# Kernel optimization log

Hardware: AMD Instinct MI355X
Metric: run time of the kernel (lower is better)

The kernel has to match this reference:

```python
import jax, jax.numpy as jnp
import numpy as np
from jax import lax

NUM_CHANNELS = 64
DILATION_DEPTH = 9
NUM_REPEAT = 2
KERNEL_SIZE = 3
DILATIONS = [2 ** d for d in range(DILATION_DEPTH)] * NUM_REPEAT  # 18 layers
B, T = 4, 32768


def causal_conv1d(x, w, b, dilation):
    # x: [B, Cin, T], w: [Cout, Cin, K], b: [Cout]
    # left-pad by (K-1)*dilation -> causal, output length T
    pad = (w.shape[-1] - 1) * dilation
    out = lax.conv_general_dilated(
        x, w, window_strides=(1,), padding=[(pad, 0)],
        rhs_dilation=(dilation,), dimension_numbers=("NCH", "OIH", "NCH"))
    return out + b[None, :, None]


def setup_inputs() -> dict:
    key = jax.random.key(0)
    ks = jax.random.split(key, 9)
    L, C = len(DILATIONS), NUM_CHANNELS
    s = 0.05
    return {
        "x": jax.random.normal(ks[0], (B, 1, T), dtype=jnp.float32),
        "in_w": jax.random.normal(ks[1], (C, 1, 1), dtype=jnp.float32) * s,
        "in_b": jax.random.normal(ks[2], (C,), dtype=jnp.float32) * s,
        "hid_w": jax.random.normal(ks[3], (L, 2 * C, C, KERNEL_SIZE), dtype=jnp.float32) * s,
        "hid_b": jax.random.normal(ks[4], (L, 2 * C), dtype=jnp.float32) * s,
        "res_w": jax.random.normal(ks[5], (L, C, C, 1), dtype=jnp.float32) * s,
        "res_b": jax.random.normal(ks[6], (L, C), dtype=jnp.float32) * s,
        "mix_w": jax.random.normal(ks[7], (1, L * C, 1), dtype=jnp.float32) * s,
        "mix_b": jax.random.normal(ks[8], (1,), dtype=jnp.float32) * s,
    }


def reference(x, in_w, in_b, hid_w, hid_b, res_w, res_b, mix_w, mix_b):
    C = NUM_CHANNELS
    out = causal_conv1d(x, in_w, in_b, 1)  # [B, C, T]
    skips = []
    for i, d in enumerate(DILATIONS):
        inp = out
        h = causal_conv1d(inp, hid_w[i], hid_b[i], d)  # [B, 2C, T]
        gated = jnp.tanh(h[:, :C]) * jax.nn.sigmoid(h[:, C:])  # [B, C, T]
        skips.append(gated)
        out = causal_conv1d(gated, res_w[i], res_b[i], 1) + inp
    skip_cat = jnp.concatenate(skips, axis=1)  # [B, L*C, T]
    return causal_conv1d(skip_cat, mix_w, mix_b, 1)  # [B, 1, T]
```

## Files before the change

kernel.cpp:

```cpp
#include <hip/hip_runtime.h>
#include <math.h>

#define T_LEN 32768
#define NB 4
#define NC 64
#define NL 18

typedef __attribute__((ext_vector_type(8))) short s16x8;
typedef __attribute__((ext_vector_type(4))) float f32x4;
#define MFMA_F16 __builtin_amdgcn_mfma_f32_16x16x32_f16

#define BAR_LGKM()                                                   \
    do {                                                             \
        asm volatile("s_waitcnt lgkmcnt(0)" ::: "memory");           \
        __builtin_amdgcn_s_barrier();                                \
        __builtin_amdgcn_sched_barrier(0);                           \
    } while (0)
#define BAR_VM(N)                                                    \
    do {                                                             \
        asm volatile("s_waitcnt vmcnt(%0) lgkmcnt(0)" ::             \
                         "i"(N) : "memory");                         \
        __builtin_amdgcn_s_barrier();                                \
        __builtin_amdgcn_sched_barrier(0);                           \
    } while (0)

__device__ inline unsigned short f2h(float f) {
    _Float16 h = (_Float16)f;
    return __builtin_bit_cast(unsigned short, h);
}
__device__ inline unsigned pack_h2(float a, float b) {
    return (unsigned)f2h(a) | ((unsigned)f2h(b) << 16);
}
__device__ inline float h2f(unsigned short u) {
    return (float)__builtin_bit_cast(_Float16, u);
}
__device__ inline float fast_sigmoid(float x) {
    return __builtin_amdgcn_rcpf(1.f + __expf(-x));
}
__device__ inline float fast_tanh(float x) {
    return 1.f - 2.f * __builtin_amdgcn_rcpf(1.f + __expf(2.f * x));
}

__global__ void prep_kernel(const float* __restrict__ hid_w,
                            const float* __restrict__ res_w,
                            const float* __restrict__ mix_b,
                            unsigned short* __restrict__ Wh,
                            unsigned short* __restrict__ Wr,
                            float* __restrict__ out,
                            float* __restrict__ zerobuf) {
    const int nW1 = NL * 128 * 192;
    const int nW2 = NL * 64 * 64;
    const int nOut = NB * T_LEN;
    const int total = nW1 + nW2 + nOut + 32;
    for (int gid = blockIdx.x * blockDim.x + threadIdx.x; gid < total;
         gid += gridDim.x * blockDim.x) {
        if (gid < nW1) {
            int K = gid % 192;
            int co = (gid / 192) & 127;
            int i = gid / (192 * 128);
            int kt = K >> 6, ci = K & 63;
            Wh[gid] = f2h(hid_w[((i * 128 + co) * 64 + ci) * 3 + kt]);
        } else if (gid < nW1 + nW2) {
            int q = gid - nW1;
            int c = q & 63, co = (q >> 6) & 63, i = q >> 12;
            Wr[q] = f2h(res_w[(i * 64 + co) * 64 + c]);
        } else if (gid < nW1 + nW2 + nOut) {
            out[gid - (nW1 + nW2)] = mix_b[0];
        } else {
            zerobuf[gid - (nW1 + nW2 + nOut)] = 0.f;
        }
    }
}

template <int DIL, bool FIRST, bool LAST>
__launch_bounds__(256, 4)
__global__ void layer_kernel(const unsigned short* __restrict__ actH,
                             unsigned short* __restrict__ outH,
                             const unsigned short* __restrict__ Wh,
                             const float* __restrict__ hb,
                             const unsigned short* __restrict__ Wr,
                             const float* __restrict__ rb,
                             const float* __restrict__ mw,
                             float* __restrict__ skip,
                             const float* __restrict__ zerobuf,
                             const float* __restrict__ x,
                             const float* __restrict__ in_w,
                             const float* __restrict__ in_b) {
    constexpr bool UNI = (DIL < 64);
    constexpr int R = UNI ? (64 + 2 * DIL) : 192;
    constexpr int SLOTS = R * 8;
    constexpr int JMAX = (SLOTS + 255) / 256;
    constexpr int GS_BASE = (UNI ? 128 : 0) * 128;
    constexpr int OUT_BASE = (UNI ? 0 : 64) * 128;
    constexpr int REG = 24576;

    __shared__ uint4 Xs[2 * 1536];
    __shared__ float Sk[256];
    char* lds = (char*)Xs;

    const int tid = threadIdx.x;
    const int w = tid >> 6;
    const int l = tid & 63;
    const int lo = l & 15;
    const int hi = l >> 4;
    const int b = blockIdx.y;
    const int tile = (blockIdx.x & 7) * 32 + (blockIdx.x >> 3);
    const int t0 = tile * 128;
    const int m0 = 16 * w;
    const int c0 = m0 + 4 * hi;

    const unsigned short* actB = actH + (size_t)b * T_LEN * NC;
    const float* xB = x + (size_t)b * T_LEN;

    s16x8 AH[2][6];
    s16x8 AR[2];
#pragma unroll
    for (int mt = 0; mt < 2; mt++) {
        const unsigned short* wp = Wh + (size_t)(m0 + 64 * mt + lo) * 192;
#pragma unroll
        for (int s = 0; s < 6; s++)
            AH[mt][s] = *(const s16x8*)(wp + 32 * s + 8 * hi);
    }
    if (!LAST) {
#pragma unroll
        for (int s = 0; s < 2; s++)
            AR[s] = *(const s16x8*)(Wr + (size_t)(m0 + lo) * 64 + 32 * s + 8 * hi);
    }
    float bA[4], bB[4], rbv[4];
#pragma unroll
    for (int r = 0; r < 4; r++) {
        bA[r] = hb[c0 + r];
        bB[r] = hb[64 + c0 + r];
        rbv[r] = LAST ? 0.f : rb[c0 + r];
    }
    const float4 mw4 = *(const float4*)(mw + c0);

    if (FIRST) {
#pragma unroll
        for (int sub = 0; sub < 2; sub++) {
            char* X = lds + sub * REG;
            const int tb = t0 + sub * 64;
#pragma unroll
            for (int j = 0; j < JMAX; j++) {
                int p = j * 256 + tid;
                if (p < SLOTS) {
                    int row = p >> 3, ch = p & 7;
                    int tg = tb + row - 2 * DIL;
                    unsigned uu[4] = {0u, 0u, 0u, 0u};
                    if (tg >= 0) {
                        float a = xB[tg];
#pragma unroll
                        for (int e = 0; e < 4; e++) {
                            float v0 = a * in_w[ch * 8 + 2 * e] + in_b[ch * 8 + 2 * e];
                            float v1 = a * in_w[ch * 8 + 2 * e + 1] + in_b[ch * 8 + 2 * e + 1];
                            uu[e] = pack_h2(v0, v1);
                        }
                    }
                    int byte = (row * 128 + ch * 16) ^ ((row & 7) << 4);
                    *(uint4*)(X + byte) = make_uint4(uu[0], uu[1], uu[2], uu[3]);
                }
            }
        }
    } else {
#pragma unroll
        for (int sub = 0; sub < 2; sub++) {
            char* X = lds + sub * REG;
            const int tb = t0 + sub * 64;
#pragma unroll
            for (int j = 0; j < JMAX; j++) {
                int s = (w * JMAX + j) * 64 + l;
                const void* src;
                if (s >= SLOTS) {
                    src = (const void*)(zerobuf + (s & 7) * 4);
                } else {
                    int row = s >> 3, ch = s & 7;
                    int chunk = ch ^ (row & 7);
                    int tg = tb + (UNI ? (row - 2 * DIL)
                                       : (((row >> 6) - 2) * DIL + (row & 63)));
                    src = (tg >= 0)
                              ? (const void*)(actB + (size_t)tg * 64 + chunk * 8)
                              : (const void*)(zerobuf + chunk * 4);
                }
                __builtin_amdgcn_global_load_lds(
                    (const __attribute__((address_space(1))) unsigned int*)src,
                    (__attribute__((address_space(3))) unsigned int*)(X +
                                                        (w * JMAX + j) * 1024),
                    16, 0, 0);
            }
        }
    }

#pragma unroll
    for (int sub = 0; sub < 2; sub++) {
        char* X = lds + sub * REG;
        const int tt0 = t0 + sub * 64;

        if (FIRST) {
            BAR_LGKM();
        } else if (sub == 0) {
            BAR_VM(JMAX);
        } else {
            BAR_VM(0);
        }

        f32x4 acc[2][4];
#pragma unroll
        for (int mt = 0; mt < 2; mt++)
#pragma unroll
            for (int nt = 0; nt < 4; nt++)
                acc[mt][nt] = (f32x4){0.f, 0.f, 0.f, 0.f};
#pragma unroll
        for (int s = 0; s < 6; s++) {
            const int tap = s >> 1, half = s & 1;
#pragma unroll
            for (int nt = 0; nt < 4; nt++) {
                int t = 16 * nt + lo;
                int row = UNI ? (t + tap * DIL) : (tap * 64 + t);
                int byte = (row * 128 + half * 64 + hi * 16) ^ ((row & 7) << 4);
                s16x8 bx = __builtin_bit_cast(s16x8, *(const uint4*)(X + byte));
                acc[0][nt] = MFMA_F16(AH[0][s], bx, acc[0][nt], 0, 0, 0);
                acc[1][nt] = MFMA_F16(AH[1][s], bx, acc[1][nt], 0, 0, 0);
            }
        }

        float4 inp[4];
        if (!LAST) {
#pragma unroll
            for (int nt = 0; nt < 4; nt++) {
                int t = 16 * nt + lo;
                int rowI = UNI ? (t + 2 * DIL) : (128 + t);
                int byteI = (rowI * 128 + c0 * 2) ^ ((rowI & 7) << 4);
                uint2 hv = *(const uint2*)(X + byteI);
                inp[nt] = make_float4(h2f((unsigned short)(hv.x & 0xffff)),
                                      h2f((unsigned short)(hv.x >> 16)),
                                      h2f((unsigned short)(hv.y & 0xffff)),
                                      h2f((unsigned short)(hv.y >> 16)));
            }
        }

        BAR_LGKM();

#pragma unroll
        for (int nt = 0; nt < 4; nt++) {
            float g[4];
#pragma unroll
            for (int r = 0; r < 4; r++) {
                float hA = acc[0][nt][r] + bA[r];
                float hB = acc[1][nt][r] + bB[r];
                g[r] = fast_tanh(hA) * fast_sigmoid(hB);
            }
            int t = 16 * nt + lo;
            if (!LAST) {
                int byte = (t * 128 + c0 * 2) ^ ((t & 7) << 4);
                *(uint2*)(X + GS_BASE + byte) =
                    make_uint2(pack_h2(g[0], g[1]), pack_h2(g[2], g[3]));
            }
            float sk = g[0] * mw4.x + g[1] * mw4.y + g[2] * mw4.z + g[3] * mw4.w;
            sk += __shfl_xor(sk, 16, 64);
            sk += __shfl_xor(sk, 32, 64);
            if (hi == 0) Sk[w * 64 + nt * 16 + lo] = sk;
        }
        BAR_LGKM();

        if (LAST) {
            if (tid < 64) {
                float s2 = Sk[tid] + Sk[64 + tid] + Sk[128 + tid] + Sk[192 + tid];
                skip[(size_t)b * T_LEN + tt0 + tid] += s2;
            }
            continue;
        }

        f32x4 acc2[4];
#pragma unroll
        for (int nt = 0; nt < 4; nt++) acc2[nt] = (f32x4){0.f, 0.f, 0.f, 0.f};
#pragma unroll
        for (int s = 0; s < 2; s++) {
#pragma unroll
            for (int nt = 0; nt < 4; nt++) {
                int t = 16 * nt + lo;
                int byte = (t * 128 + s * 64 + hi * 16) ^ ((t & 7) << 4);
                s16x8 bg = __builtin_bit_cast(
                    s16x8, *(const uint4*)(X + GS_BASE + byte));
                acc2[nt] = MFMA_F16(AR[s], bg, acc2[nt], 0, 0, 0);
            }
        }

        char* OutH = X + OUT_BASE;
#pragma unroll
        for (int nt = 0; nt < 4; nt++) {
            int t = 16 * nt + lo;
            float ox = acc2[nt][0] + rbv[0] + inp[nt].x;
            float oy = acc2[nt][1] + rbv[1] + inp[nt].y;
            float oz = acc2[nt][2] + rbv[2] + inp[nt].z;
            float ow = acc2[nt][3] + rbv[3] + inp[nt].w;
            int byteB = (t * 128 + c0 * 2) ^ ((t & 7) << 4);
            *(uint2*)(OutH + byteB) =
                make_uint2(pack_h2(ox, oy), pack_h2(oz, ow));
        }

        if (tid < 64) {
            float s2 = Sk[tid] + Sk[64 + tid] + Sk[128 + tid] + Sk[192 + tid];
            skip[(size_t)b * T_LEN + tt0 + tid] += s2;
        }
        BAR_LGKM();

        unsigned short* gH = outH + (size_t)b * T_LEN * NC + (size_t)tt0 * 64;
#pragma unroll
        for (int i = 0; i < 2; i++) {
            int u = i * 256 + tid;
            int t = u >> 3, ch = u & 7;
            uint4 v = *(const uint4*)(OutH + t * 128 + ((ch ^ (t & 7)) << 4));
            ((uint4*)gH)[u] = v;
        }
    }
}

extern "C" void kernel_launch(void* const* d_in, const int* in_sizes, int n_in,
                              void* d_out, int out_size, void* d_ws, size_t ws_size,
                              hipStream_t stream) {
    const float* x     = (const float*)d_in[0];
    const float* in_w  = (const float*)d_in[1];
    const float* in_b  = (const float*)d_in[2];
    const float* hid_w = (const float*)d_in[3];
    const float* hid_b = (const float*)d_in[4];
    const float* res_w = (const float*)d_in[5];
    const float* res_b = (const float*)d_in[6];
    const float* mix_w = (const float*)d_in[7];
    const float* mix_b = (const float*)d_in[8];
    float* out = (float*)d_out;

    const size_t actN = (size_t)NB * T_LEN * NC;
    unsigned short* H0 = (unsigned short*)d_ws;
    unsigned short* H1 = H0 + actN;
    unsigned short* Wh = H1 + actN;
    unsigned short* Wr = Wh + (size_t)NL * 128 * 192;
    float* zerobuf = (float*)(Wr + (size_t)NL * 64 * 64);

    prep_kernel<<<512, 256, 0, stream>>>(hid_w, res_w, mix_b, Wh, Wr, out,
                                         zerobuf);

    static const int dils[NL] = {1, 2, 4, 8, 16, 32, 64, 128, 256,
                                 1, 2, 4, 8, 16, 32, 64, 128, 256};
    const unsigned short* srcH = H0;
    unsigned short* dstH = H1;
    dim3 grid(T_LEN / 128, NB);

#define LL(D, F, L)                                                           \
    layer_kernel<D, F, L><<<grid, 256, 0, stream>>>(                          \
        srcH, dstH, Wh + (size_t)i * 128 * 192, hid_b + (size_t)i * 128,      \
        Wr + (size_t)i * 64 * 64, res_b + (size_t)i * 64,                     \
        mix_w + (size_t)i * 64, out, zerobuf, x, in_w, in_b)

    for (int i = 0; i < NL; i++) {
        if (i == 0) {
            LL(1, true, false);
        } else if (i == NL - 1) {
            LL(256, false, true);
        } else {
            switch (dils[i]) {
                case 1:   LL(1, false, false);   break;
                case 2:   LL(2, false, false);   break;
                case 4:   LL(4, false, false);   break;
                case 8:   LL(8, false, false);   break;
                case 16:  LL(16, false, false);  break;
                case 32:  LL(32, false, false);  break;
                case 64:  LL(64, false, false);  break;
                case 128: LL(128, false, false); break;
                case 256: LL(256, false, false); break;
            }
        }
        const unsigned short* tH = srcH; srcH = dstH; dstH = (unsigned short*)tH;
    }
#undef LL
}
```

Baseline: 373.9 us.

## Loop each block over the batch with double-buffered async staging

Each block now handles one 64-step time tile for all four batch elements instead of two time sub-tiles of one batch. While the current batch element is computed, the global-to-LDS load for the next one is issued into the other LDS buffer. Weight register loads are amortised over more work per block, and the grid shrinks from 1024 to 512 blocks. Extra barriers are added at the end of each iteration so the ping-pong buffer is safe to reuse, and the lower block count may reduce latency hiding.

```diff
diff --git a/kernel.cpp b/kernel.cpp
--- a/kernel.cpp
+++ b/kernel.cpp
@@ -103,14 +103,13 @@
     const int l = tid & 63;
     const int lo = l & 15;
     const int hi = l >> 4;
-    const int b = blockIdx.y;
-    const int tile = (blockIdx.x & 7) * 32 + (blockIdx.x >> 3);
-    const int t0 = tile * 128;
+    const int blk = blockIdx.x;
+    const int tile = (blk & 7) * 64 + (blk >> 3);
+    const int t0 = tile * 64;
     const int m0 = 16 * w;
     const int c0 = m0 + 4 * hi;
 
-    const unsigned short* actB = actH + (size_t)b * T_LEN * NC;
-    const float* xB = x + (size_t)b * T_LEN;
+    const float* xB0 = x;
 
     s16x8 AH[2][6];
     s16x8 AR[2];
@@ -135,73 +134,70 @@
     }
     const float4 mw4 = *(const float4*)(mw + c0);
 
-    if (FIRST) {
-#pragma unroll
-        for (int sub = 0; sub < 2; sub++) {
-            char* X = lds + sub * REG;
-            const int tb = t0 + sub * 64;
-#pragma unroll
-            for (int j = 0; j < JMAX; j++) {
-                int p = j * 256 + tid;
-                if (p < SLOTS) {
-                    int row = p >> 3, ch = p & 7;
-                    int tg = tb + row - 2 * DIL;
-                    unsigned uu[4] = {0u, 0u, 0u, 0u};
-                    if (tg >= 0) {
-                        float a = xB[tg];
-#pragma unroll
-                        for (int e = 0; e < 4; e++) {
-                            float v0 = a * in_w[ch * 8 + 2 * e] + in_b[ch * 8 + 2 * e];
-                            float v1 = a * in_w[ch * 8 + 2 * e + 1] + in_b[ch * 8 + 2 * e + 1];
-                            uu[e] = pack_h2(v0, v1);
-                        }
+    auto stage_async = [&](int bb, char* X) {
+        const unsigned short* aB = actH + (size_t)bb * T_LEN * NC;
+#pragma unroll
+        for (int jj = 0; jj < JMAX; jj++) {
+            int s = (w * JMAX + jj) * 64 + l;
+            const void* src;
+            if (s >= SLOTS) {
+                src = (const void*)(zerobuf + (s & 7) * 4);
+            } else {
+                int row = s >> 3, ch = s & 7;
+                int chunk = ch ^ (row & 7);
+                int tg = t0 + (UNI ? (row - 2 * DIL)
+                                   : (((row >> 6) - 2) * DIL + (row & 63)));
+                src = (tg >= 0)
+                          ? (const void*)(aB + (size_t)tg * 64 + chunk * 8)
+                          : (const void*)(zerobuf + chunk * 4);
+            }
+            __builtin_amdgcn_global_load_lds(
+                (const __attribute__((address_space(1))) unsigned int*)src,
+                (__attribute__((address_space(3))) unsigned int*)(X +
+                                                        (w * JMAX + jj) * 1024),
+                16, 0, 0);
+        }
+    };
+    auto stage_first = [&](int bb, char* X) {
+        const float* xB = xB0 + (size_t)bb * T_LEN;
+#pragma unroll
+        for (int jj = 0; jj < JMAX; jj++) {
+            int p = jj * 256 + tid;
+            if (p < SLOTS) {
+                int row = p >> 3, ch = p & 7;
+                int tg = t0 + row - 2 * DIL;
+                unsigned uu[4] = {0u, 0u, 0u, 0u};
+                if (tg >= 0) {
+                    float a = xB[tg];
+#pragma unroll
+                    for (int e = 0; e < 4; e++) {
+                        float v0 = a * in_w[ch * 8 + 2 * e] + in_b[ch * 8 + 2 * e];
+                        float v1 = a * in_w[ch * 8 + 2 * e + 1] + in_b[ch * 8 + 2 * e + 1];
+                        uu[e] = pack_h2(v0, v1);
                     }
-                    int byte = (row * 128 + ch * 16) ^ ((row & 7) << 4);
-                    *(uint4*)(X + byte) = make_uint4(uu[0], uu[1], uu[2], uu[3]);
                 }
-            }
-        }
-    } else {
-#pragma unroll
-        for (int sub = 0; sub < 2; sub++) {
-            char* X = lds + sub * REG;
-            const int tb = t0 + sub * 64;
-#pragma unroll
-            for (int j = 0; j < JMAX; j++) {
-                int s = (w * JMAX + j) * 64 + l;
-                const void* src;
-                if (s >= SLOTS) {
-                    src = (const void*)(zerobuf + (s & 7) * 4);
-                } else {
-                    int row = s >> 3, ch = s & 7;
-                    int chunk = ch ^ (row & 7);
-                    int tg = tb + (UNI ? (row - 2 * DIL)
-                                       : (((row >> 6) - 2) * DIL + (row & 63)));
-                    src = (tg >= 0)
-                              ? (const void*)(actB + (size_t)tg * 64 + chunk * 8)
-                              : (const void*)(zerobuf + chunk * 4);
-                }
-                __builtin_amdgcn_global_load_lds(
-                    (const __attribute__((address_space(1))) unsigned int*)src,
-                    (__attribute__((address_space(3))) unsigned int*)(X +
-                                                        (w * JMAX + j) * 1024),
-                    16, 0, 0);
-            }
-        }
-    }
-
-#pragma unroll
-    for (int sub = 0; sub < 2; sub++) {
-        char* X = lds + sub * REG;
-        const int tt0 = t0 + sub * 64;
-
-        if (FIRST) {
-            BAR_LGKM();
-        } else if (sub == 0) {
-            BAR_VM(JMAX);
-        } else {
-            BAR_VM(0);
-        }
+                int byte = (row * 128 + ch * 16) ^ ((row & 7) << 4);
+                *(uint4*)(X + byte) = make_uint4(uu[0], uu[1], uu[2], uu[3]);
+            }
+        }
+    };
+
+    if (FIRST) stage_first(0, lds);
+    else       stage_async(0, lds);
+
+#pragma unroll
+    for (int j = 0; j < NB; j++) {
+        char* X = lds + (j & 1) * REG;
+        const int b = j;
+
+        if (j + 1 < NB) {
+            if (FIRST) stage_first(j + 1, lds + ((j + 1) & 1) * REG);
+            else       stage_async(j + 1, lds + ((j + 1) & 1) * REG);
+        }
+
+        if (FIRST)          BAR_LGKM();
+        else if (j + 1 < NB) BAR_VM(JMAX);
+        else                 BAR_VM(0);
 
         f32x4 acc[2][4];
 #pragma unroll
@@ -265,8 +261,9 @@
         if (LAST) {
             if (tid < 64) {
                 float s2 = Sk[tid] + Sk[64 + tid] + Sk[128 + tid] + Sk[192 + tid];
-                skip[(size_t)b * T_LEN + tt0 + tid] += s2;
-            }
+                skip[(size_t)b * T_LEN + t0 + tid] += s2;
+            }
+            BAR_LGKM();
             continue;
         }
 
@@ -300,11 +297,11 @@
 
         if (tid < 64) {
             float s2 = Sk[tid] + Sk[64 + tid] + Sk[128 + tid] + Sk[192 + tid];
-            skip[(size_t)b * T_LEN + tt0 + tid] += s2;
+            skip[(size_t)b * T_LEN + t0 + tid] += s2;
         }
         BAR_LGKM();
 
-        unsigned short* gH = outH + (size_t)b * T_LEN * NC + (size_t)tt0 * 64;
+        unsigned short* gH = outH + (size_t)b * T_LEN * NC + (size_t)t0 * 64;
 #pragma unroll
         for (int i = 0; i < 2; i++) {
             int u = i * 256 + tid;
@@ -312,6 +309,7 @@
             uint4 v = *(const uint4*)(OutH + t * 128 + ((ch ^ (t & 7)) << 4));
             ((uint4*)gH)[u] = v;
         }
+        BAR_LGKM();
     }
 }
 
@@ -343,10 +341,9 @@
                                  1, 2, 4, 8, 16, 32, 64, 128, 256};
     const unsigned short* srcH = H0;
     unsigned short* dstH = H1;
-    dim3 grid(T_LEN / 128, NB);
 
 #define LL(D, F, L)                                                           \
-    layer_kernel<D, F, L><<<grid, 256, 0, stream>>>(                          \
+    layer_kernel<D, F, L><<<512, 256, 0, stream>>>(                           \
         srcH, dstH, Wh + (size_t)i * 128 * 192, hid_b + (size_t)i * 128,      \
         Wr + (size_t)i * 64 * 64, res_b + (size_t)i * 64,                     \
         mix_w + (size_t)i * 64, out, zerobuf, x, in_w, in_b)
```

Result: faster. 349.1 us (-6.6%).
